# Kernel optimization log

Hardware: AMD Instinct MI355X
Metric: run time of the kernel (lower is better)

## Reference

```python
import jax, jax.numpy as jnp
import numpy as np

B, T, D_IN = 64, 1024, 12
H = 256          # hidden_dim
N_CLASSES = 17


def _lstm_dir(x, w_ih, w_hh, b_ih, b_hh, reverse):
    """Single-direction LSTM. x: [B,T,D]; w_ih: [4H,D]; w_hh: [4H,H]. Returns [B,T,H].
    Gate order follows PyTorch: i, f, g, o."""
    # Precompute input projection for all timesteps (big GEMM, compute-friendly)
    x_proj = jnp.einsum('btd,gd->btg', x, w_ih) + (b_ih + b_hh)  # [B,T,4H]
    x_proj = jnp.swapaxes(x_proj, 0, 1)  # [T,B,4H]
    h0 = jnp.zeros((x.shape[0], H), x.dtype)
    c0 = jnp.zeros((x.shape[0], H), x.dtype)

    def step(carry, xt):
        h, c = carry
        gates = xt + h @ w_hh.T  # [B,4H]
        i, f, g, o = jnp.split(gates, 4, axis=-1)
        c = jax.nn.sigmoid(f) * c + jax.nn.sigmoid(i) * jnp.tanh(g)
        h = jax.nn.sigmoid(o) * jnp.tanh(c)
        return (h, c), h

    _, hs = jax.lax.scan(step, (h0, c0), x_proj, reverse=reverse)  # hs: [T,B,H]
    return jnp.swapaxes(hs, 0, 1)  # [B,T,H]


def _bilstm_layer(x, w_ih, w_hh, b_ih, b_hh):
    """w_*: stacked [2, ...] for (forward, backward) directions."""
    fwd = _lstm_dir(x, w_ih[0], w_hh[0], b_ih[0], b_hh[0], reverse=False)
    bwd = _lstm_dir(x, w_ih[1], w_hh[1], b_ih[1], b_hh[1], reverse=True)
    return jnp.concatenate([fwd, bwd], axis=-1)  # [B,T,2H]


def setup_inputs() -> dict:
    key = jax.random.key(0)
    ks = jax.random.split(key, 11)
    s = 1.0 / np.sqrt(H)  # PyTorch LSTM init scale
    x = jax.random.normal(ks[0], (B, T, D_IN), dtype=jnp.float32)
    # Layer 0: input dim D_IN; Layer 1: input dim 2H (bidirectional outputs)
    w_ih0 = jax.random.uniform(ks[1], (2, 4 * H, D_IN), minval=-s, maxval=s)
    w_hh0 = jax.random.uniform(ks[2], (2, 4 * H, H), minval=-s, maxval=s)
    b_ih0 = jax.random.uniform(ks[3], (2, 4 * H), minval=-s, maxval=s)
    b_hh0 = jax.random.uniform(ks[4], (2, 4 * H), minval=-s, maxval=s)
    w_ih1 = jax.random.uniform(ks[5], (2, 4 * H, 2 * H), minval=-s, maxval=s)
    w_hh1 = jax.random.uniform(ks[6], (2, 4 * H, H), minval=-s, maxval=s)
    b_ih1 = jax.random.uniform(ks[7], (2, 4 * H), minval=-s, maxval=s)
    b_hh1 = jax.random.uniform(ks[8], (2, 4 * H), minval=-s, maxval=s)
    fc_w = jax.random.uniform(ks[9], (N_CLASSES, 2 * H), minval=-s, maxval=s)
    fc_b = jax.random.uniform(ks[10], (N_CLASSES,), minval=-s, maxval=s)
    return {"x": x, "w_ih0": w_ih0, "w_hh0": w_hh0, "b_ih0": b_ih0, "b_hh0": b_hh0,
            "w_ih1": w_ih1, "w_hh1": w_hh1, "b_ih1": b_ih1, "b_hh1": b_hh1,
            "fc_w": fc_w, "fc_b": fc_b}


def reference(x, w_ih0, w_hh0, b_ih0, b_hh0, w_ih1, w_hh1, b_ih1, b_hh1, fc_w, fc_b):
    # Eval mode: dropout layers are identity.
    h = _bilstm_layer(x, w_ih0, w_hh0, b_ih0, b_hh0)   # [B,T,2H]
    h = _bilstm_layer(h, w_ih1, w_hh1, b_ih1, b_hh1)   # [B,T,2H]
    pooled = h.mean(axis=1)                             # [B,2H]
    return pooled @ fc_w.T + fc_b                       # [B,n_classes]
```

## Files before the change

### kernel.cpp

```cpp
#include <hip/hip_runtime.h>

#define NB 64
#define NT 1024
#define DIN 12
#define NH 256
#define NG 1024
#define NCLS 17
#define TCL 128
#define NCHUNK 8
#define XPS ((size_t)2 * NB * TCL * NG)

typedef _Float16 f16;
typedef __attribute__((ext_vector_type(2))) _Float16 half2_t;
typedef __attribute__((ext_vector_type(8))) _Float16 f16x8;
typedef __attribute__((ext_vector_type(4))) float f32x4;
typedef unsigned int uint;
typedef unsigned short ushort;

__device__ __forceinline__ float sigm(float v) { return 1.0f / (1.0f + __expf(-v)); }
__device__ __forceinline__ float tanh_(float v) {
    v = fminf(fmaxf(v, -15.0f), 15.0f);
    float e = __expf(2.0f * v);
    return (e - 1.0f) / (e + 1.0f);
}
__device__ __forceinline__ float dot2(uint w, uint h, float c) {
    return __builtin_amdgcn_fdot2(__builtin_bit_cast(half2_t, w),
                                  __builtin_bit_cast(half2_t, h), c, false);
}
__device__ __forceinline__ uint pack16(float a, float b) {
    union { f16 h[2]; uint u; } cv; cv.h[0] = (f16)a; cv.h[1] = (f16)b; return cv.u;
}
__device__ __forceinline__ uint pkrtz(float a, float b) {
    return __builtin_bit_cast(uint, __builtin_amdgcn_cvt_pkrtz(a, b));
}
__device__ __forceinline__ ushort hbits(f16 v) {
    union { f16 h; ushort u; } cv; cv.h = v; return cv.u;
}
__device__ __forceinline__ uint rdlane(uint v, int l) {
    return (uint)__builtin_amdgcn_readlane((int)v, l);
}

__global__ void k_prep(const float* __restrict__ w_hh0, const float* __restrict__ w_hh1,
                       const float* __restrict__ w_ih0, const float* __restrict__ w_ih1,
                       const float* __restrict__ b_ih1, const float* __restrict__ b_hh1,
                       uint* __restrict__ Wkv0, uint* __restrict__ Wka0,
                       uint* __restrict__ Wkl0, uint* __restrict__ wih0p,
                       uint* __restrict__ Wkv1, uint* __restrict__ Wka1,
                       uint* __restrict__ Wkl1,
                       f16* __restrict__ wih1h, float* __restrict__ bsum1) {
    int i = blockIdx.x * 256 + threadIdx.x;
    if (i < 2 * 4 * 256 * 40) {
        int kp = i % 40; int r = i / 40;
        int t = r & 255, q = (r >> 8) & 3, dir = r >> 10;
        const float* row = w_hh0 + (size_t)dir * NG * NH + (size_t)(q * 256 + t) * NH;
        Wkv0[i] = pack16(row[2 * kp], row[2 * kp + 1]);
    }
    if (i < 2 * 4 * 256 * 60) {
        int kp = 40 + (i % 60); int r = i / 60;
        int t = r & 255, q = (r >> 8) & 3, dir = r >> 10;
        const float* row = w_hh0 + (size_t)dir * NG * NH + (size_t)(q * 256 + t) * NH;
        Wka0[i] = pack16(row[2 * kp], row[2 * kp + 1]);
    }
    if (i < 2 * 4 * 7 * 256 * 4) {
        int j = i & 3; int u = i >> 2;
        int t = u & 255; int v = u >> 8;
        int g = v % 7; int w2 = v / 7;
        int q = w2 & 3, dir = w2 >> 2;
        int kp = 100 + 4 * g + j;
        const float* row = w_hh0 + (size_t)dir * NG * NH + (size_t)(q * 256 + t) * NH;
        Wkl0[i] = pack16(row[2 * kp], row[2 * kp + 1]);
    }
    if (i < 2 * 4 * 6 * 256) {
        int t = i & 255; int r = i >> 8;
        int dp = r % 6, q = (r / 6) & 3, dd = r / 24;
        const float* row = w_ih0 + ((size_t)dd * NG + q * 256 + t) * DIN;
        wih0p[i] = pack16(row[2 * dp], row[2 * dp + 1]);
    }
    if (i < 2 * 4 * 256 * 48) {
        int kp = i % 48; int r = i / 48;
        int t = r & 255, q = (r >> 8) & 3, dir = r >> 10;
        const float* row = w_hh1 + (size_t)dir * NG * NH + (size_t)(q * 256 + t) * NH;
        Wkv1[i] = pack16(row[2 * kp], row[2 * kp + 1]);
    }
    if (i < 2 * 4 * 256 * 60) {
        int kp = 48 + (i % 60); int r = i / 60;
        int t = r & 255, q = (r >> 8) & 3, dir = r >> 10;
        const float* row = w_hh1 + (size_t)dir * NG * NH + (size_t)(q * 256 + t) * NH;
        Wka1[i] = pack16(row[2 * kp], row[2 * kp + 1]);
    }
    if (i < 2 * 4 * 5 * 256 * 4) {
        int j = i & 3; int u = i >> 2;
        int t = u & 255; int v = u >> 8;
        int g = v % 5; int w2 = v / 5;
        int q = w2 & 3, dir = w2 >> 2;
        int kp = 108 + 4 * g + j;
        const float* row = w_hh1 + (size_t)dir * NG * NH + (size_t)(q * 256 + t) * NH;
        Wkl1[i] = pack16(row[2 * kp], row[2 * kp + 1]);
    }
    if (i < 2 * NG * 2 * NH) wih1h[i] = (f16)w_ih1[i];
    if (i < 2 * NG) bsum1[i] = b_ih1[i] + b_hh1[i];
}

__device__ void rec0_seq(char* smem, int rb,
                         const uint* __restrict__ Wkv0, const uint* __restrict__ Wka0,
                         const uint4* __restrict__ Wkl0, const uint* __restrict__ wih0p,
                         const float* __restrict__ b_ih0, const float* __restrict__ b_hh0,
                         const float* __restrict__ x, f16* __restrict__ out0h,
                         float* __restrict__ hst, float* __restrict__ cst) {
    uint4* wlds4 = (uint4*)smem;
    ushort* hs16 = (ushort*)(smem + 114688);

    const int tid = threadIdx.x;
    const int dir = rb >> 6;
    const int b = rb & 63;

    for (int n = tid; n < 7168; n += 256) wlds4[n] = Wkl0[dir * 7168 + n];

    uint4 wrv[4][10];
    #pragma unroll
    for (int q = 0; q < 4; ++q) {
        const uint* src = Wkv0 + (size_t)((dir * 4 + q) * 256 + tid) * 40;
        #pragma unroll
        for (int m = 0; m < 10; ++m) wrv[q][m] = *(const uint4*)(src + m * 4);
    }

    uint aw[240];
    #pragma unroll
    for (int q = 0; q < 4; ++q) {
        const uint* src = Wka0 + (size_t)((dir * 4 + q) * 256 + tid) * 60;
        #pragma unroll
        for (int m = 0; m < 15; ++m) {
            uint4 v = *(const uint4*)(src + m * 4);
            asm volatile("v_accvgpr_write_b32 %0, %1" : "=a"(aw[(q * 15 + m) * 4 + 0]) : "v"(v.x));
            asm volatile("v_accvgpr_write_b32 %0, %1" : "=a"(aw[(q * 15 + m) * 4 + 1]) : "v"(v.y));
            asm volatile("v_accvgpr_write_b32 %0, %1" : "=a"(aw[(q * 15 + m) * 4 + 2]) : "v"(v.z));
            asm volatile("v_accvgpr_write_b32 %0, %1" : "=a"(aw[(q * 15 + m) * 4 + 3]) : "v"(v.w));
        }
    }

    uint wihr[24];
    float bias[4];
    #pragma unroll
    for (int q = 0; q < 4; ++q) {
        #pragma unroll
        for (int dp = 0; dp < 6; ++dp)
            wihr[q * 6 + dp] = wih0p[((dir * 4 + q) * 6 + dp) * 256 + tid];
        bias[q] = b_ih0[dir * NG + q * 256 + tid] + b_hh0[dir * NG + q * 256 + tid];
    }

    const int sidx = (dir * NB + b) * NH + tid;
    float cv = 0.f, hv = 0.f;
    hs16[tid] = hbits((f16)0.f);
    __syncthreads();

    #pragma unroll 1
    for (int it = 0; it < NT; ++it) {
        const int par = it & 1;
        uint4 hvv = ((const uint4*)(hs16 + par * 256))[tid & 31];

        float ah[4] = {0.f, 0.f, 0.f, 0.f};

        const int t = dir ? (NT - 1 - it) : it;
        const float4* xp = (const float4*)(x + ((size_t)b * NT + t) * DIN);
        float4 A = xp[0], B4 = xp[1], C4 = xp[2];
        float xv[12] = {A.x, A.y, A.z, A.w, B4.x, B4.y, B4.z, B4.w,
                        C4.x, C4.y, C4.z, C4.w};

        #pragma unroll
        for (int g8 = 0; g8 < 10; ++g8) {
            uint s0 = rdlane(hvv.x, g8), s1 = rdlane(hvv.y, g8);
            uint s2 = rdlane(hvv.z, g8), s3 = rdlane(hvv.w, g8);
            #pragma unroll
            for (int q = 0; q < 4; ++q) {
                uint4 w = wrv[q][g8];
                ah[q] = dot2(w.x, s0, ah[q]);
                ah[q] = dot2(w.y, s1, ah[q]);
                ah[q] = dot2(w.z, s2, ah[q]);
                ah[q] = dot2(w.w, s3, ah[q]);
            }
        }
        #pragma unroll
        for (int m = 0; m < 15; ++m) {
            const int g8 = 10 + m;
            uint s0 = rdlane(hvv.x, g8), s1 = rdlane(hvv.y, g8);
            uint s2 = rdlane(hvv.z, g8), s3 = rdlane(hvv.w, g8);
            #pragma unroll
            for (int q = 0; q < 4; ++q) {
                uint w0, w1, w2, w3;
                asm volatile("v_accvgpr_read_b32 %0, %1" : "=v"(w0) : "a"(aw[(q * 15 + m) * 4 + 0]));
                asm volatile("v_accvgpr_read_b32 %0, %1" : "=v"(w1) : "a"(aw[(q * 15 + m) * 4 + 1]));
                asm volatile("v_accvgpr_read_b32 %0, %1" : "=v"(w2) : "a"(aw[(q * 15 + m) * 4 + 2]));
                asm volatile("v_accvgpr_read_b32 %0, %1" : "=v"(w3) : "a"(aw[(q * 15 + m) * 4 + 3]));
                ah[q] = dot2(w0, s0, ah[q]);
                ah[q] = dot2(w1, s1, ah[q]);
                ah[q] = dot2(w2, s2, ah[q]);
                ah[q] = dot2(w3, s3, ah[q]);
            }
        }
        #pragma unroll
        for (int g = 0; g < 7; ++g) {
            const int g8 = 25 + g;
            uint s0 = rdlane(hvv.x, g8), s1 = rdlane(hvv.y, g8);
            uint s2 = rdlane(hvv.z, g8), s3 = rdlane(hvv.w, g8);
            #pragma unroll
            for (int q = 0; q < 4; ++q) {
                uint4 w = wlds4[(q * 7 + g) * 256 + tid];
                ah[q] = dot2(w.x, s0, ah[q]);
                ah[q] = dot2(w.y, s1, ah[q]);
                ah[q] = dot2(w.z, s2, ah[q]);
                ah[q] = dot2(w.w, s3, ah[q]);
            }
        }

        float z[4];
        uint xph[6];
        #pragma unroll
        for (int d = 0; d < 6; ++d) xph[d] = pkrtz(xv[2 * d], xv[2 * d + 1]);
        #pragma unroll
        for (int q = 0; q < 4; ++q) {
            float a = bias[q];
            #pragma unroll
            for (int d = 0; d < 6; ++d)
                a = dot2(wihr[q * 6 + d], xph[d], a);
            z[q] = ah[q] + a;
        }
        cv = sigm(z[1]) * cv + sigm(z[0]) * tanh_(z[2]);
        hv = sigm(z[3]) * tanh_(cv);

        f16 hi = (f16)hv;
        hs16[(par ^ 1) * 256 + tid] = hbits(hi);
        out0h[((size_t)b * NT + t) * 512 + dir * 256 + tid] = hi;
        __syncthreads();
    }

    cst[sidx] = cv; hst[sidx] = hv;
}

__device__ void rec1_seq(char* smem, int rb, int chunk, int nsteps,
                         const uint* __restrict__ Wkv1, const uint* __restrict__ Wka1,
                         const uint4* __restrict__ Wkl1, const float* __restrict__ xp1,
                         float* __restrict__ hst, float* __restrict__ cst,
                         float* __restrict__ hsm) {
    uint4* wlds4 = (uint4*)smem;
    ushort* hs16 = (ushort*)(smem + 81920);

    const int tid = threadIdx.x;
    const int dir = rb >> 6;
    const int b = rb & 63;
    const int ld = 2 + dir;

    for (int n = tid; n < 5120; n += 256) wlds4[n] = Wkl1[dir * 5120 + n];

    uint4 wrv[4][12];
    #pragma unroll
    for (int q = 0; q < 4; ++q) {
        const uint* src = Wkv1 + (size_t)((dir * 4 + q) * 256 + tid) * 48;
        #pragma unroll
        for (int m = 0; m < 12; ++m) wrv[q][m] = *(const uint4*)(src + m * 4);
    }

    uint aw[240];
    #pragma unroll
    for (int q = 0; q < 4; ++q) {
        const uint* src = Wka1 + (size_t)((dir * 4 + q) * 256 + tid) * 60;
        #pragma unroll
        for (int m = 0; m < 15; ++m) {
            uint4 v = *(const uint4*)(src + m * 4);
            asm volatile("v_accvgpr_write_b32 %0, %1" : "=a"(aw[(q * 15 + m) * 4 + 0]) : "v"(v.x));
            asm volatile("v_accvgpr_write_b32 %0, %1" : "=a"(aw[(q * 15 + m) * 4 + 1]) : "v"(v.y));
            asm volatile("v_accvgpr_write_b32 %0, %1" : "=a"(aw[(q * 15 + m) * 4 + 2]) : "v"(v.z));
            asm volatile("v_accvgpr_write_b32 %0, %1" : "=a"(aw[(q * 15 + m) * 4 + 3]) : "v"(v.w));
        }
    }

    const int sidx = (ld * NB + b) * NH + tid;
    float cv, hv, hsv = 0.f;
    if (chunk == 0) { cv = 0.f; hv = 0.f; }
    else {
        cv = cst[sidx]; hv = hst[sidx];
        hsv = hsm[(dir * NB + b) * NH + tid];
    }
    hs16[tid] = hbits((f16)hv);

    const float* xbase = xp1 + ((size_t)dir * NB + b) * TCL * NG + tid * 4;
    float4 xq_cur = *(const float4*)xbase;
    __syncthreads();

    #pragma unroll 1
    for (int it = 0; it < nsteps; ++it) {
        const int par = it & 1;
        const uint4* Hh = (const uint4*)(hs16 + par * 256);

        const int itn = (it + 1 < nsteps) ? (it + 1) : it;
        float4 xq_nxt = *(const float4*)(xbase + (size_t)itn * NG);

        float ah[4] = {0.f, 0.f, 0.f, 0.f};

        #pragma unroll
        for (int g8 = 0; g8 < 12; ++g8) {
            uint4 H = Hh[g8];
            #pragma unroll
            for (int q = 0; q < 4; ++q) {
                uint4 w = wrv[q][g8];
                ah[q] = dot2(w.x, H.x, ah[q]);
                ah[q] = dot2(w.y, H.y, ah[q]);
                ah[q] = dot2(w.z, H.z, ah[q]);
                ah[q] = dot2(w.w, H.w, ah[q]);
            }
        }
        #pragma unroll
        for (int m = 0; m < 15; ++m) {
            const int g8 = 12 + m;
            uint4 H = Hh[g8];
            #pragma unroll
            for (int q = 0; q < 4; ++q) {
                uint w0, w1, w2, w3;
                asm volatile("v_accvgpr_read_b32 %0, %1" : "=v"(w0) : "a"(aw[(q * 15 + m) * 4 + 0]));
                asm volatile("v_accvgpr_read_b32 %0, %1" : "=v"(w1) : "a"(aw[(q * 15 + m) * 4 + 1]));
                asm volatile("v_accvgpr_read_b32 %0, %1" : "=v"(w2) : "a"(aw[(q * 15 + m) * 4 + 2]));
                asm volatile("v_accvgpr_read_b32 %0, %1" : "=v"(w3) : "a"(aw[(q * 15 + m) * 4 + 3]));
                ah[q] = dot2(w0, H.x, ah[q]);
                ah[q] = dot2(w1, H.y, ah[q]);
                ah[q] = dot2(w2, H.z, ah[q]);
                ah[q] = dot2(w3, H.w, ah[q]);
            }
        }
        #pragma unroll
        for (int g = 0; g < 5; ++g) {
            const int g8 = 27 + g;
            uint4 H = Hh[g8];
            #pragma unroll
            for (int q = 0; q < 4; ++q) {
                uint4 w = wlds4[(q * 5 + g) * 256 + tid];
                ah[q] = dot2(w.x, H.x, ah[q]);
                ah[q] = dot2(w.y, H.y, ah[q]);
                ah[q] = dot2(w.z, H.z, ah[q]);
                ah[q] = dot2(w.w, H.w, ah[q]);
            }
        }

        float z0 = ah[0] + xq_cur.x;
        float z1 = ah[1] + xq_cur.y;
        float z2 = ah[2] + xq_cur.z;
        float z3 = ah[3] + xq_cur.w;
        cv = sigm(z1) * cv + sigm(z0) * tanh_(z2);
        hv = sigm(z3) * tanh_(cv);
        hsv += hv;

        hs16[(par ^ 1) * 256 + tid] = hbits((f16)hv);
        __syncthreads();
        xq_cur = xq_nxt;
    }

    cst[sidx] = cv; hst[sidx] = hv;
    hsm[(dir * NB + b) * NH + tid] = hsv;
}

__device__ void proj_role(int pb, int c,
                          const f16* __restrict__ out0h, const f16* __restrict__ wih1h,
                          const float* __restrict__ bsum1, float* __restrict__ xp1) {
    const int tid = threadIdx.x;
    const int w = tid >> 6, l = tid & 63;
    const int lane16 = l & 15, quad = l >> 4;

    #pragma unroll 1
    for (int mi = 0; mi < 2; ++mi) {
        const int mtg = pb * 8 + w * 2 + mi;
        const int dirt = mtg >> 9;
        const int mtl = mtg & 511;

        const int ra = mtl * 16 + lane16;
        const int ab = ra >> 7, tla = ra & 127;
        const int ta = dirt ? (NT - 1 - c * TCL - tla) : (c * TCL + tla);
        const f16* Arow = out0h + ((size_t)ab * NT + ta) * 512 + quad * 8;

        uint4 afr[16];
        #pragma unroll
        for (int kt = 0; kt < 16; ++kt) afr[kt] = *(const uint4*)(Arow + kt * 32);

        int ob[4], otl[4];
        #pragma unroll
        for (int reg = 0; reg < 4; ++reg) {
            int rr = mtl * 16 + quad * 4 + reg;
            ob[reg] = rr >> 7; otl[reg] = rr & 127;
        }

        const f16* Bbase = wih1h + (size_t)dirt * NG * 512 + quad * 8;

        #pragma unroll 1
        for (int nt = 0; nt < 64; ++nt) {
            const int col = nt * 16 + lane16;
            const f16* Brow = Bbase + (size_t)col * 512;
            float bias = bsum1[dirt * NG + col];

            f32x4 acc = {0.f, 0.f, 0.f, 0.f};
            #pragma unroll
            for (int kt = 0; kt < 16; ++kt) {
                uint4 bv = *(const uint4*)(Brow + kt * 32);
                acc = __builtin_amdgcn_mfma_f32_16x16x32_f16(
                    __builtin_bit_cast(f16x8, afr[kt]),
                    __builtin_bit_cast(f16x8, bv), acc, 0, 0, 0);
            }
            const int ucol = col & 255, qcol = col >> 8;
            #pragma unroll
            for (int reg = 0; reg < 4; ++reg) {
                xp1[((size_t)(dirt * NB + ob[reg]) * TCL + otl[reg]) * NG
                    + ucol * 4 + qcol] = acc[reg] + bias;
            }
        }
    }
}

__global__ __launch_bounds__(256, 1) void k_rec0(
    const uint* __restrict__ Wkv0, const uint* __restrict__ Wka0,
    const uint4* __restrict__ Wkl0, const uint* __restrict__ wih0p,
    const float* __restrict__ b_ih0, const float* __restrict__ b_hh0,
    const float* __restrict__ x, f16* __restrict__ out0h,
    float* __restrict__ hst, float* __restrict__ cst) {
    extern __shared__ __align__(16) char smem[];
    rec0_seq(smem, blockIdx.x, Wkv0, Wka0, Wkl0, wih0p, b_ih0, b_hh0,
             x, out0h, hst, cst);
}

__global__ __launch_bounds__(256, 1) void k_pipe(
    int j,
    const uint* __restrict__ Wkv1, const uint* __restrict__ Wka1,
    const uint4* __restrict__ Wkl1,
    const f16* __restrict__ out0h, const f16* __restrict__ wih1h,
    const float* __restrict__ bsum1, float* __restrict__ xp1,
    float* __restrict__ hst, float* __restrict__ cst, float* __restrict__ hsm) {
    extern __shared__ __align__(16) char smem[];
    const int bid = blockIdx.x;
    if (bid < 128) {
        const int cc = j - 1;
        if (cc >= 0 && cc < NCHUNK)
            rec1_seq(smem, bid, cc, TCL, Wkv1, Wka1, Wkl1,
                     xp1 + (size_t)(cc & 1) * XPS, hst, cst, hsm);
    } else {
        const int cp = j;
        if (cp < NCHUNK)
            proj_role(bid - 128, cp, out0h, wih1h, bsum1,
                      xp1 + (size_t)(cp & 1) * XPS);
    }
}

__global__ void k_fc(const float* __restrict__ hsm, const float* __restrict__ fc_w,
                     const float* __restrict__ fc_b, float* __restrict__ out) {
    const int b = blockIdx.x;
    const int n = threadIdx.x;
    if (n >= NCLS) return;
    float acc = fc_b[n];
    const float inv = 1.0f / (float)NT;
    for (int k = 0; k < 2 * NH; ++k) {
        float pv = hsm[((k >> 8) * NB + b) * NH + (k & 255)];
        acc += (pv * inv) * fc_w[n * 2 * NH + k];
    }
    out[b * NCLS + n] = acc;
}

extern "C" void kernel_launch(void* const* d_in, const int* in_sizes, int n_in,
                              void* d_out, int out_size, void* d_ws, size_t ws_size,
                              hipStream_t stream) {
    const float* x     = (const float*)d_in[0];
    const float* w_ih0 = (const float*)d_in[1];
    const float* w_hh0 = (const float*)d_in[2];
    const float* b_ih0 = (const float*)d_in[3];
    const float* b_hh0 = (const float*)d_in[4];
    const float* w_ih1 = (const float*)d_in[5];
    const float* w_hh1 = (const float*)d_in[6];
    const float* b_ih1 = (const float*)d_in[7];
    const float* b_hh1 = (const float*)d_in[8];
    const float* fc_w  = (const float*)d_in[9];
    const float* fc_b  = (const float*)d_in[10];
    float* out = (float*)d_out;

    char* ws = (char*)d_ws;
    uint* Wkv0  = (uint*)ws;
    uint* Wka0  = Wkv0 + 81920;
    uint* Wkl0  = Wka0 + 122880;
    uint* wih0p = Wkl0 + 57344;
    uint* Wkv1  = wih0p + 12288;
    uint* Wka1  = Wkv1 + 98304;
    uint* Wkl1  = Wka1 + 122880;
    f16* wih1h  = (f16*)(Wkl1 + 40960);
    float* bsum1 = (float*)(wih1h + 1048576);
    float* hst  = bsum1 + 2048;
    float* cst  = hst + 65536;
    float* hsm  = cst + 65536;
    float* xp1  = hsm + 32768;
    f16* out0h  = (f16*)(xp1 + 2 * XPS);

    k_prep<<<dim3(4096), dim3(256), 0, stream>>>(
        w_hh0, w_hh1, w_ih0, w_ih1, b_ih1, b_hh1,
        Wkv0, Wka0, Wkl0, wih0p, Wkv1, Wka1, Wkl1, wih1h, bsum1);

    k_rec0<<<dim3(128), dim3(256), 115712, stream>>>(
        Wkv0, Wka0, (const uint4*)Wkl0, wih0p, b_ih0, b_hh0, x, out0h, hst, cst);

    for (int j = 0; j <= NCHUNK; ++j) {
        k_pipe<<<dim3(256), dim3(256), 82944, stream>>>(
            j, Wkv1, Wka1, (const uint4*)Wkl1, out0h, wih1h, bsum1,
            xp1, hst, cst, hsm);
    }

    k_fc<<<dim3(64), dim3(32), 0, stream>>>(hsm, fc_w, fc_b, out);
}
```

Before: 4.690 ms.

## Rebalance LSTM recurrent weights across VGPR/AGPR/LDS and software-pipeline LDS loads

Changes how the recurrent weight matrix is split between register storage (VGPR and AGPR) and LDS. Layer 0 moves one group from VGPRs to AGPRs, and layer 1 shrinks its LDS share so AGPRs hold 16 groups. The LDS-resident weight loads are now double-buffered and interleaved with the AGPR dot-product groups so LDS latency is hidden behind register math. Layer 1 also switches from per-group LDS reads of h to one LDS load plus readlane broadcasts, and the k_pipe LDS footprint drops. The risks are higher register pressure and possible spills.

```diff
diff --git a/kernel.cpp b/kernel.cpp
--- a/kernel.cpp
+++ b/kernel.cpp
@@ -49,14 +49,14 @@
                        uint* __restrict__ Wkl1,
                        f16* __restrict__ wih1h, float* __restrict__ bsum1) {
     int i = blockIdx.x * 256 + threadIdx.x;
-    if (i < 2 * 4 * 256 * 40) {
-        int kp = i % 40; int r = i / 40;
+    if (i < 2 * 4 * 256 * 36) {
+        int kp = i % 36; int r = i / 36;
         int t = r & 255, q = (r >> 8) & 3, dir = r >> 10;
         const float* row = w_hh0 + (size_t)dir * NG * NH + (size_t)(q * 256 + t) * NH;
         Wkv0[i] = pack16(row[2 * kp], row[2 * kp + 1]);
     }
-    if (i < 2 * 4 * 256 * 60) {
-        int kp = 40 + (i % 60); int r = i / 60;
+    if (i < 2 * 4 * 256 * 64) {
+        int kp = 36 + (i % 64); int r = i / 64;
         int t = r & 255, q = (r >> 8) & 3, dir = r >> 10;
         const float* row = w_hh0 + (size_t)dir * NG * NH + (size_t)(q * 256 + t) * NH;
         Wka0[i] = pack16(row[2 * kp], row[2 * kp + 1]);
@@ -82,24 +82,64 @@
         const float* row = w_hh1 + (size_t)dir * NG * NH + (size_t)(q * 256 + t) * NH;
         Wkv1[i] = pack16(row[2 * kp], row[2 * kp + 1]);
     }
-    if (i < 2 * 4 * 256 * 60) {
-        int kp = 48 + (i % 60); int r = i / 60;
+    if (i < 2 * 4 * 256 * 64) {
+        int kp = 48 + (i % 64); int r = i / 64;
         int t = r & 255, q = (r >> 8) & 3, dir = r >> 10;
         const float* row = w_hh1 + (size_t)dir * NG * NH + (size_t)(q * 256 + t) * NH;
         Wka1[i] = pack16(row[2 * kp], row[2 * kp + 1]);
     }
-    if (i < 2 * 4 * 5 * 256 * 4) {
+    if (i < 2 * 4 * 4 * 256 * 4) {
         int j = i & 3; int u = i >> 2;
         int t = u & 255; int v = u >> 8;
-        int g = v % 5; int w2 = v / 5;
+        int g = v & 3; int w2 = v >> 2;
         int q = w2 & 3, dir = w2 >> 2;
-        int kp = 108 + 4 * g + j;
+        int kp = 112 + 4 * g + j;
         const float* row = w_hh1 + (size_t)dir * NG * NH + (size_t)(q * 256 + t) * NH;
         Wkl1[i] = pack16(row[2 * kp], row[2 * kp + 1]);
     }
     if (i < 2 * NG * 2 * NH) wih1h[i] = (f16)w_ih1[i];
     if (i < 2 * NG) bsum1[i] = b_ih1[i] + b_hh1[i];
 }
+
+#define VGRP(g8) { \
+    uint s0 = rdlane(hvv.x, g8), s1 = rdlane(hvv.y, g8); \
+    uint s2 = rdlane(hvv.z, g8), s3 = rdlane(hvv.w, g8); \
+    _Pragma("unroll") for (int q = 0; q < 4; ++q) { \
+        uint4 w = wrv[q][g8]; \
+        ah[q] = dot2(w.x, s0, ah[q]); \
+        ah[q] = dot2(w.y, s1, ah[q]); \
+        ah[q] = dot2(w.z, s2, ah[q]); \
+        ah[q] = dot2(w.w, s3, ah[q]); } }
+
+#define AGRP(m, G8B) { \
+    const int g8 = (G8B) + (m); \
+    uint s0 = rdlane(hvv.x, g8), s1 = rdlane(hvv.y, g8); \
+    uint s2 = rdlane(hvv.z, g8), s3 = rdlane(hvv.w, g8); \
+    _Pragma("unroll") for (int q = 0; q < 4; ++q) { \
+        uint w0, w1, w2, w3; \
+        asm volatile("v_accvgpr_read_b32 %0, %1" : "=v"(w0) : "a"(aw[(q * 16 + (m)) * 4 + 0])); \
+        asm volatile("v_accvgpr_read_b32 %0, %1" : "=v"(w1) : "a"(aw[(q * 16 + (m)) * 4 + 1])); \
+        asm volatile("v_accvgpr_read_b32 %0, %1" : "=v"(w2) : "a"(aw[(q * 16 + (m)) * 4 + 2])); \
+        asm volatile("v_accvgpr_read_b32 %0, %1" : "=v"(w3) : "a"(aw[(q * 16 + (m)) * 4 + 3])); \
+        ah[q] = dot2(w0, s0, ah[q]); \
+        ah[q] = dot2(w1, s1, ah[q]); \
+        ah[q] = dot2(w2, s2, ah[q]); \
+        ah[q] = dot2(w3, s3, ah[q]); } }
+
+#define LISS(slot, g, NGRP) { \
+    _Pragma("unroll") for (int q = 0; q < 4; ++q) \
+        lw[slot][q] = wlds4[(q * (NGRP) + (g)) * 256 + tid]; }
+
+#define LCON(slot, g, G8B) { \
+    const int g8 = (G8B) + (g); \
+    uint s0 = rdlane(hvv.x, g8), s1 = rdlane(hvv.y, g8); \
+    uint s2 = rdlane(hvv.z, g8), s3 = rdlane(hvv.w, g8); \
+    _Pragma("unroll") for (int q = 0; q < 4; ++q) { \
+        uint4 w = lw[slot][q]; \
+        ah[q] = dot2(w.x, s0, ah[q]); \
+        ah[q] = dot2(w.y, s1, ah[q]); \
+        ah[q] = dot2(w.z, s2, ah[q]); \
+        ah[q] = dot2(w.w, s3, ah[q]); } }
 
 __device__ void rec0_seq(char* smem, int rb,
                          const uint* __restrict__ Wkv0, const uint* __restrict__ Wka0,
@@ -116,25 +156,25 @@
 
     for (int n = tid; n < 7168; n += 256) wlds4[n] = Wkl0[dir * 7168 + n];
 
-    uint4 wrv[4][10];
+    uint4 wrv[4][9];
     #pragma unroll
     for (int q = 0; q < 4; ++q) {
-        const uint* src = Wkv0 + (size_t)((dir * 4 + q) * 256 + tid) * 40;
-        #pragma unroll
-        for (int m = 0; m < 10; ++m) wrv[q][m] = *(const uint4*)(src + m * 4);
-    }
-
-    uint aw[240];
+        const uint* src = Wkv0 + (size_t)((dir * 4 + q) * 256 + tid) * 36;
+        #pragma unroll
+        for (int m = 0; m < 9; ++m) wrv[q][m] = *(const uint4*)(src + m * 4);
+    }
+
+    uint aw[256];
     #pragma unroll
     for (int q = 0; q < 4; ++q) {
-        const uint* src = Wka0 + (size_t)((dir * 4 + q) * 256 + tid) * 60;
-        #pragma unroll
-        for (int m = 0; m < 15; ++m) {
+        const uint* src = Wka0 + (size_t)((dir * 4 + q) * 256 + tid) * 64;
+        #pragma unroll
+        for (int m = 0; m < 16; ++m) {
             uint4 v = *(const uint4*)(src + m * 4);
-            asm volatile("v_accvgpr_write_b32 %0, %1" : "=a"(aw[(q * 15 + m) * 4 + 0]) : "v"(v.x));
-            asm volatile("v_accvgpr_write_b32 %0, %1" : "=a"(aw[(q * 15 + m) * 4 + 1]) : "v"(v.y));
-            asm volatile("v_accvgpr_write_b32 %0, %1" : "=a"(aw[(q * 15 + m) * 4 + 2]) : "v"(v.z));
-            asm volatile("v_accvgpr_write_b32 %0, %1" : "=a"(aw[(q * 15 + m) * 4 + 3]) : "v"(v.w));
+            asm volatile("v_accvgpr_write_b32 %0, %1" : "=a"(aw[(q * 16 + m) * 4 + 0]) : "v"(v.x));
+            asm volatile("v_accvgpr_write_b32 %0, %1" : "=a"(aw[(q * 16 + m) * 4 + 1]) : "v"(v.y));
+            asm volatile("v_accvgpr_write_b32 %0, %1" : "=a"(aw[(q * 16 + m) * 4 + 2]) : "v"(v.z));
+            asm volatile("v_accvgpr_write_b32 %0, %1" : "=a"(aw[(q * 16 + m) * 4 + 3]) : "v"(v.w));
         }
     }
 
@@ -152,6 +192,9 @@
     float cv = 0.f, hv = 0.f;
     hs16[tid] = hbits((f16)0.f);
     __syncthreads();
+
+    uint4 lw[2][4];
+    LISS(0, 0, 7) LISS(1, 1, 7)
 
     #pragma unroll 1
     for (int it = 0; it < NT; ++it) {
@@ -166,51 +209,22 @@
         float xv[12] = {A.x, A.y, A.z, A.w, B4.x, B4.y, B4.z, B4.w,
                         C4.x, C4.y, C4.z, C4.w};
 
-        #pragma unroll
-        for (int g8 = 0; g8 < 10; ++g8) {
-            uint s0 = rdlane(hvv.x, g8), s1 = rdlane(hvv.y, g8);
-            uint s2 = rdlane(hvv.z, g8), s3 = rdlane(hvv.w, g8);
-            #pragma unroll
-            for (int q = 0; q < 4; ++q) {
-                uint4 w = wrv[q][g8];
-                ah[q] = dot2(w.x, s0, ah[q]);
-                ah[q] = dot2(w.y, s1, ah[q]);
-                ah[q] = dot2(w.z, s2, ah[q]);
-                ah[q] = dot2(w.w, s3, ah[q]);
-            }
-        }
-        #pragma unroll
-        for (int m = 0; m < 15; ++m) {
-            const int g8 = 10 + m;
-            uint s0 = rdlane(hvv.x, g8), s1 = rdlane(hvv.y, g8);
-            uint s2 = rdlane(hvv.z, g8), s3 = rdlane(hvv.w, g8);
-            #pragma unroll
-            for (int q = 0; q < 4; ++q) {
-                uint w0, w1, w2, w3;
-                asm volatile("v_accvgpr_read_b32 %0, %1" : "=v"(w0) : "a"(aw[(q * 15 + m) * 4 + 0]));
-                asm volatile("v_accvgpr_read_b32 %0, %1" : "=v"(w1) : "a"(aw[(q * 15 + m) * 4 + 1]));
-                asm volatile("v_accvgpr_read_b32 %0, %1" : "=v"(w2) : "a"(aw[(q * 15 + m) * 4 + 2]));
-                asm volatile("v_accvgpr_read_b32 %0, %1" : "=v"(w3) : "a"(aw[(q * 15 + m) * 4 + 3]));
-                ah[q] = dot2(w0, s0, ah[q]);
-                ah[q] = dot2(w1, s1, ah[q]);
-                ah[q] = dot2(w2, s2, ah[q]);
-                ah[q] = dot2(w3, s3, ah[q]);
-            }
-        }
-        #pragma unroll
-        for (int g = 0; g < 7; ++g) {
-            const int g8 = 25 + g;
-            uint s0 = rdlane(hvv.x, g8), s1 = rdlane(hvv.y, g8);
-            uint s2 = rdlane(hvv.z, g8), s3 = rdlane(hvv.w, g8);
-            #pragma unroll
-            for (int q = 0; q < 4; ++q) {
-                uint4 w = wlds4[(q * 7 + g) * 256 + tid];
-                ah[q] = dot2(w.x, s0, ah[q]);
-                ah[q] = dot2(w.y, s1, ah[q]);
-                ah[q] = dot2(w.z, s2, ah[q]);
-                ah[q] = dot2(w.w, s3, ah[q]);
-            }
-        }
+        VGRP(0) VGRP(1) VGRP(2) VGRP(3) VGRP(4)
+        VGRP(5) VGRP(6) VGRP(7) VGRP(8)
+        LCON(0, 0, 25) LISS(0, 2, 7)
+        AGRP(0, 9) AGRP(1, 9) AGRP(2, 9)
+        LCON(1, 1, 25) LISS(1, 3, 7)
+        AGRP(3, 9) AGRP(4, 9) AGRP(5, 9)
+        LCON(0, 2, 25) LISS(0, 4, 7)
+        AGRP(6, 9) AGRP(7, 9) AGRP(8, 9)
+        LCON(1, 3, 25) LISS(1, 5, 7)
+        AGRP(9, 9) AGRP(10, 9) AGRP(11, 9)
+        LCON(0, 4, 25) LISS(0, 6, 7)
+        AGRP(12, 9) AGRP(13, 9)
+        LCON(1, 5, 25)
+        AGRP(14, 9) AGRP(15, 9)
+        LCON(0, 6, 25)
+        LISS(0, 0, 7) LISS(1, 1, 7)
 
         float z[4];
         uint xph[6];
@@ -242,14 +256,14 @@
                          float* __restrict__ hst, float* __restrict__ cst,
                          float* __restrict__ hsm) {
     uint4* wlds4 = (uint4*)smem;
-    ushort* hs16 = (ushort*)(smem + 81920);
+    ushort* hs16 = (ushort*)(smem + 65536);
 
     const int tid = threadIdx.x;
     const int dir = rb >> 6;
     const int b = rb & 63;
     const int ld = 2 + dir;
 
-    for (int n = tid; n < 5120; n += 256) wlds4[n] = Wkl1[dir * 5120 + n];
+    for (int n = tid; n < 4096; n += 256) wlds4[n] = Wkl1[dir * 4096 + n];
 
     uint4 wrv[4][12];
     #pragma unroll
@@ -259,17 +273,17 @@
         for (int m = 0; m < 12; ++m) wrv[q][m] = *(const uint4*)(src + m * 4);
     }
 
-    uint aw[240];
+    uint aw[256];
     #pragma unroll
     for (int q = 0; q < 4; ++q) {
-        const uint* src = Wka1 + (size_t)((dir * 4 + q) * 256 + tid) * 60;
-        #pragma unroll
-        for (int m = 0; m < 15; ++m) {
+        const uint* src = Wka1 + (size_t)((dir * 4 + q) * 256 + tid) * 64;
+        #pragma unroll
+        for (int m = 0; m < 16; ++m) {
             uint4 v = *(const uint4*)(src + m * 4);
-            asm volatile("v_accvgpr_write_b32 %0, %1" : "=a"(aw[(q * 15 + m) * 4 + 0]) : "v"(v.x));
-            asm volatile("v_accvgpr_write_b32 %0, %1" : "=a"(aw[(q * 15 + m) * 4 + 1]) : "v"(v.y));
-            asm volatile("v_accvgpr_write_b32 %0, %1" : "=a"(aw[(q * 15 + m) * 4 + 2]) : "v"(v.z));
-            asm volatile("v_accvgpr_write_b32 %0, %1" : "=a"(aw[(q * 15 + m) * 4 + 3]) : "v"(v.w));
+            asm volatile("v_accvgpr_write_b32 %0, %1" : "=a"(aw[(q * 16 + m) * 4 + 0]) : "v"(v.x));
+            asm volatile("v_accvgpr_write_b32 %0, %1" : "=a"(aw[(q * 16 + m) * 4 + 1]) : "v"(v.y));
+            asm volatile("v_accvgpr_write_b32 %0, %1" : "=a"(aw[(q * 16 + m) * 4 + 2]) : "v"(v.z));
+            asm volatile("v_accvgpr_write_b32 %0, %1" : "=a"(aw[(q * 16 + m) * 4 + 3]) : "v"(v.w));
         }
     }
 
@@ -286,58 +300,30 @@
     float4 xq_cur = *(const float4*)xbase;
     __syncthreads();
 
+    uint4 lw[2][4];
+    LISS(0, 0, 4) LISS(1, 1, 4)
+
     #pragma unroll 1
     for (int it = 0; it < nsteps; ++it) {
         const int par = it & 1;
-        const uint4* Hh = (const uint4*)(hs16 + par * 256);
+        uint4 hvv = ((const uint4*)(hs16 + par * 256))[tid & 31];
 
         const int itn = (it + 1 < nsteps) ? (it + 1) : it;
         float4 xq_nxt = *(const float4*)(xbase + (size_t)itn * NG);
 
         float ah[4] = {0.f, 0.f, 0.f, 0.f};
 
-        #pragma unroll
-        for (int g8 = 0; g8 < 12; ++g8) {
-            uint4 H = Hh[g8];
-            #pragma unroll
-            for (int q = 0; q < 4; ++q) {
-                uint4 w = wrv[q][g8];
-                ah[q] = dot2(w.x, H.x, ah[q]);
-                ah[q] = dot2(w.y, H.y, ah[q]);
-                ah[q] = dot2(w.z, H.z, ah[q]);
-                ah[q] = dot2(w.w, H.w, ah[q]);
-            }
-        }
-        #pragma unroll
-        for (int m = 0; m < 15; ++m) {
-            const int g8 = 12 + m;
-            uint4 H = Hh[g8];
-            #pragma unroll
-            for (int q = 0; q < 4; ++q) {
-                uint w0, w1, w2, w3;
-                asm volatile("v_accvgpr_read_b32 %0, %1" : "=v"(w0) : "a"(aw[(q * 15 + m) * 4 + 0]));
-                asm volatile("v_accvgpr_read_b32 %0, %1" : "=v"(w1) : "a"(aw[(q * 15 + m) * 4 + 1]));
-                asm volatile("v_accvgpr_read_b32 %0, %1" : "=v"(w2) : "a"(aw[(q * 15 + m) * 4 + 2]));
-                asm volatile("v_accvgpr_read_b32 %0, %1" : "=v"(w3) : "a"(aw[(q * 15 + m) * 4 + 3]));
-                ah[q] = dot2(w0, H.x, ah[q]);
-                ah[q] = dot2(w1, H.y, ah[q]);
-                ah[q] = dot2(w2, H.z, ah[q]);
-                ah[q] = dot2(w3, H.w, ah[q]);
-            }
-        }
-        #pragma unroll
-        for (int g = 0; g < 5; ++g) {
-            const int g8 = 27 + g;
-            uint4 H = Hh[g8];
-            #pragma unroll
-            for (int q = 0; q < 4; ++q) {
-                uint4 w = wlds4[(q * 5 + g) * 256 + tid];
-                ah[q] = dot2(w.x, H.x, ah[q]);
-                ah[q] = dot2(w.y, H.y, ah[q]);
-                ah[q] = dot2(w.z, H.z, ah[q]);
-                ah[q] = dot2(w.w, H.w, ah[q]);
-            }
-        }
+        VGRP(0) VGRP(1) VGRP(2) VGRP(3) VGRP(4) VGRP(5)
+        VGRP(6) VGRP(7) VGRP(8) VGRP(9) VGRP(10) VGRP(11)
+        LCON(0, 0, 28) LISS(0, 2, 4)
+        AGRP(0, 12) AGRP(1, 12) AGRP(2, 12) AGRP(3, 12) AGRP(4, 12)
+        LCON(1, 1, 28) LISS(1, 3, 4)
+        AGRP(5, 12) AGRP(6, 12) AGRP(7, 12) AGRP(8, 12) AGRP(9, 12)
+        LCON(0, 2, 28)
+        AGRP(10, 12) AGRP(11, 12) AGRP(12, 12) AGRP(13, 12) AGRP(14, 12)
+        LCON(1, 3, 28)
+        AGRP(15, 12)
+        LISS(0, 0, 4) LISS(1, 1, 4)
 
         float z0 = ah[0] + xq_cur.x;
         float z1 = ah[1] + xq_cur.y;
@@ -476,13 +462,13 @@
 
     char* ws = (char*)d_ws;
     uint* Wkv0  = (uint*)ws;
-    uint* Wka0  = Wkv0 + 81920;
-    uint* Wkl0  = Wka0 + 122880;
+    uint* Wka0  = Wkv0 + 73728;
+    uint* Wkl0  = Wka0 + 131072;
     uint* wih0p = Wkl0 + 57344;
     uint* Wkv1  = wih0p + 12288;
     uint* Wka1  = Wkv1 + 98304;
-    uint* Wkl1  = Wka1 + 122880;
-    f16* wih1h  = (f16*)(Wkl1 + 40960);
+    uint* Wkl1  = Wka1 + 131072;
+    f16* wih1h  = (f16*)(Wkl1 + 32768);
     float* bsum1 = (float*)(wih1h + 1048576);
     float* hst  = bsum1 + 2048;
     float* cst  = hst + 65536;
@@ -498,7 +484,7 @@
         Wkv0, Wka0, (const uint4*)Wkl0, wih0p, b_ih0, b_hh0, x, out0h, hst, cst);
 
     for (int j = 0; j <= NCHUNK; ++j) {
-        k_pipe<<<dim3(256), dim3(256), 82944, stream>>>(
+        k_pipe<<<dim3(256), dim3(256), 66560, stream>>>(
             j, Wkv1, Wka1, (const uint4*)Wkl1, out0h, wih1h, bsum1,
             xp1, hst, cst, hsm);
     }
```

Measured after the change: 5.056 ms. 7.8% more time.
